# Kernel tuning notes

Hardware: AMD Instinct MI355X
Metric: run time of the kernel (lower is better)

## Reference

```python
import jax, jax.numpy as jnp
import numpy as np

NUM_HEADS = 32
MAX_BIAS_LENGTH = 1024
ROPE_BASE = 10000.0


def _rope_cos_sin(seq_len, head_dim, dtype):
    half = head_dim // 2
    inv_freq = 1.0 / (ROPE_BASE ** (jnp.arange(0, half, dtype=jnp.float32) / half))
    t = jnp.arange(seq_len, dtype=jnp.float32)
    freqs = jnp.outer(t, inv_freq)  # [S, half]
    return jnp.cos(freqs).astype(dtype), jnp.sin(freqs).astype(dtype)


def _apply_rope(x, cos, sin):
    # x: [B, S, H, D]; non-interleaved (GPT-NeoX / flash-attn style) rotary
    half = x.shape[-1] // 2
    x1, x2 = x[..., :half], x[..., half:]
    c = cos[None, :, None, :]
    s = sin[None, :, None, :]
    return jnp.concatenate([x1 * c - x2 * s, x1 * s + x2 * c], axis=-1)


def setup_inputs() -> dict:
    key = jax.random.key(0)
    ks = jax.random.split(key, 7)
    B, S, Dm = 2, 2048, 2048
    std = 1.0 / np.sqrt(Dm)
    return {
        "hidden_states": jax.random.normal(ks[0], (B, S, Dm), jnp.float32),
        "Wq": jax.random.normal(ks[1], (Dm, Dm), jnp.float32) * std,
        "Wk": jax.random.normal(ks[2], (Dm, Dm), jnp.float32) * std,
        "Wv": jax.random.normal(ks[3], (Dm, Dm), jnp.float32) * std,
        "Wo": jax.random.normal(ks[4], (Dm, Dm), jnp.float32) * std,
        "learnable_bias": jax.random.normal(ks[5], (NUM_HEADS, MAX_BIAS_LENGTH), jnp.float32) * 0.001,
        "softmax_offset": jnp.zeros((NUM_HEADS,), jnp.float32),
    }


def reference(hidden_states, Wq, Wk, Wv, Wo, learnable_bias, softmax_offset):
    B, S, Dm = hidden_states.shape
    H = NUM_HEADS
    D = Dm // H
    scale = D ** -0.5

    # projections (nn.Linear: x @ W.T)
    q = (hidden_states @ Wq.T).reshape(B, S, H, D)
    k = (hidden_states @ Wk.T).reshape(B, S, H, D)
    v = (hidden_states @ Wv.T).reshape(B, S, H, D)

    cos, sin = _rope_cos_sin(S, D, q.dtype)
    q = _apply_rope(q, cos, sin)
    k = _apply_rope(k, cos, sin)

    q = q.transpose(0, 2, 1, 3)  # [B, H, S, D]
    k = k.transpose(0, 2, 1, 3)
    v = v.transpose(0, 2, 1, 3)

    scores = jnp.einsum("bhid,bhjd->bhij", q, k) * scale  # [B, H, S, S]

    # per-diagonal learnable bias: diag = i - j in [0, MAX_BIAS_LENGTH)
    i = jnp.arange(S)[:, None]
    j = jnp.arange(S)[None, :]
    diag = i - j  # [S, S]
    causal = diag >= 0
    in_band = causal & (diag < MAX_BIAS_LENGTH)
    bias = jnp.where(in_band, learnable_bias[:, jnp.clip(diag, 0, MAX_BIAS_LENGTH - 1)], 0.0)  # [H, S, S]
    scores = scores + bias[None]
    scores = jnp.where(causal[None, None], scores, -jnp.inf)

    # softmax with learnable per-head offset (attention-sink logit)
    off = softmax_offset[None, :, None]  # [1, H, 1]
    m = jnp.maximum(jnp.max(scores, axis=-1), off)  # [B, H, S]
    p = jnp.exp(scores - m[..., None])
    denom = jnp.sum(p, axis=-1) + jnp.exp(off - m)  # [B, H, S]
    out = jnp.einsum("bhij,bhjd->bhid", p, v) / denom[..., None]

    out = out.transpose(0, 2, 1, 3).reshape(B, S, Dm)
    return out @ Wo.T
```

## Files before the change

kernel.cpp:

```cpp
#include <hip/hip_runtime.h>
#include <hip/hip_bf16.h>
#include <stdint.h>

typedef __bf16 bf16x8 __attribute__((ext_vector_type(8)));
typedef float f32x4 __attribute__((ext_vector_type(4)));
typedef unsigned short u16;
typedef u16 u16x4 __attribute__((ext_vector_type(4)));

#define S_LEN 2048
#define DMODEL 2048
#define NHEADS 32
#define BATCH 2
#define MROWS (BATCH * S_LEN)
#define BIAS_LEN 1024
#define LOG2E 1.44269504088896f

__device__ __forceinline__ u16 b16(float f) {
  union { __bf16 h; u16 u; } cv; cv.h = (__bf16)f; return cv.u;
}

__device__ __forceinline__ void gload16(const void* g, void* l) {
  __builtin_amdgcn_global_load_lds(
      (const __attribute__((address_space(1))) uint32_t*)g,
      (__attribute__((address_space(3))) uint32_t*)l, 16, 0, 0);
}

__global__ __launch_bounds__(256)
void prep_all(const float* __restrict__ hs,
              const float* __restrict__ w0, const float* __restrict__ w1,
              const float* __restrict__ w2, const float* __restrict__ w3,
              const float* __restrict__ bias,
              u16* __restrict__ hs_b, u16* __restrict__ w_b,
              float* __restrict__ ct, float* __restrict__ st,
              u16* __restrict__ b16t)
{
  const int blk = blockIdx.x;
  if (blk < 8192) {
    int i = (blk * 256 + threadIdx.x) * 4;
    float4 v = *(const float4*)(hs + i);
    u16x4 o = { b16(v.x), b16(v.y), b16(v.z), b16(v.w) };
    *(u16x4*)(hs_b + i) = o;
  } else if (blk < 24576) {
    int r = blk - 8192;
    int which = r >> 12;
    const float* src = (which == 0) ? w0 : (which == 1) ? w1
                     : (which == 2) ? w2 : w3;
    int i = ((r & 4095) * 256 + threadIdx.x) * 4;
    float4 v = *(const float4*)(src + i);
    u16x4 o = { b16(v.x), b16(v.y), b16(v.z), b16(v.w) };
    *(u16x4*)(w_b + (size_t)which * DMODEL * DMODEL + i) = o;
  } else if (blk < 24832) {
    int idx = (blk - 24576) * 256 + threadIdx.x;
    int s = idx >> 5, d = idx & 31;
    float inv = exp2f((float)d * (-13.287712379549449f / 32.0f));
    float a = (float)s * inv;
    ct[idx] = cosf(a);
    st[idx] = sinf(a);
  } else {
    int i = (blk - 24832) * 256 + threadIdx.x;
    b16t[i] = b16(bias[i] * LOG2E);
  }
}

#define GEMM_MAIN_LOOP(Aptr, Bptr)                                            \
  f32x4 acc[4][4] = {};                                                       \
  const u16* aS[4]; const u16* bS[4];                                         \
  _Pragma("unroll")                                                           \
  for (int it = 0; it < 4; ++it) {                                            \
    int u = it * 256 + tid;                                                   \
    int row = u >> 3;                                                         \
    int ch  = (u & 7) ^ (row & 7);                                            \
    aS[it] = (Aptr) + (size_t)(tm + row) * DMODEL + ch * 8;                   \
    bS[it] = (Bptr) + (size_t)(tn + row) * DMODEL + ch * 8;                   \
  }                                                                           \
  for (int k0 = 0; k0 < DMODEL; k0 += 64) {                                   \
    __syncthreads();                                                          \
    _Pragma("unroll")                                                         \
    for (int it = 0; it < 4; ++it) {                                          \
      int u = it * 256 + tid;                                                 \
      gload16(aS[it] + k0, (char*)sA + u * 16);                               \
      gload16(bS[it] + k0, (char*)sB + u * 16);                               \
    }                                                                         \
    __syncthreads();                                                          \
    _Pragma("unroll")                                                         \
    for (int kk = 0; kk < 2; ++kk) {                                          \
      bf16x8 af[4], bq[4];                                                    \
      _Pragma("unroll")                                                       \
      for (int mi = 0; mi < 4; ++mi) {                                        \
        int row = wm * 64 + mi * 16 + lc;                                     \
        int ch  = (kk * 4 + lr) ^ (row & 7);                                  \
        af[mi] = *(const bf16x8*)((const char*)sA + row * 128 + ch * 16);     \
      }                                                                       \
      _Pragma("unroll")                                                       \
      for (int ni = 0; ni < 4; ++ni) {                                        \
        int row = wn * 64 + ni * 16 + lc;                                     \
        int ch  = (kk * 4 + lr) ^ (row & 7);                                  \
        bq[ni] = *(const bf16x8*)((const char*)sB + row * 128 + ch * 16);     \
      }                                                                       \
      _Pragma("unroll")                                                       \
      for (int mi = 0; mi < 4; ++mi)                                          \
        _Pragma("unroll")                                                     \
        for (int ni = 0; ni < 4; ++ni)                                        \
          acc[mi][ni] = __builtin_amdgcn_mfma_f32_16x16x32_bf16(              \
              af[mi], bq[ni], acc[mi][ni], 0, 0, 0);                          \
    }                                                                         \
  }

__global__ __launch_bounds__(256)
void gemm_qkv(const u16* __restrict__ A, const u16* __restrict__ W,
              u16* __restrict__ qf, u16* __restrict__ kf, u16* __restrict__ vt,
              const float* __restrict__ ctab, const float* __restrict__ stab)
{
  __shared__ u16 sA[128 * 64];
  __shared__ u16 sB[128 * 64];
  const int tid  = threadIdx.x;
  const int lane = tid & 63;
  const int wid  = tid >> 6;
  const int wm   = wid >> 1, wn = wid & 1;
  const int lc   = lane & 15, lr = lane >> 4;
  const int L = blockIdx.x;
  const int r = L >> 3;
  const int x = (L & 7) * 6 + (r % 6);
  const int y = r / 6;
  const int which = x >> 4;
  const int tn = (x & 15) * 128;
  const int tm = y * 128;
  const u16* Bm = W + (size_t)which * DMODEL * DMODEL;

  GEMM_MAIN_LOOP(A, Bm)

  if (which == 2) {
    u16* C = vt;
#pragma unroll
    for (int mi = 0; mi < 4; ++mi)
#pragma unroll
      for (int ni = 0; ni < 4; ++ni) {
        int col = tn + wn * 64 + ni * 16 + lc;
        int hh = col >> 6, d = col & 63;
        int m0 = tm + wm * 64 + mi * 16 + lr * 4;
        int bb = m0 >> 11, s = m0 & 2047;
        u16x4 v = { b16(acc[mi][ni][0]), b16(acc[mi][ni][1]),
                    b16(acc[mi][ni][2]), b16(acc[mi][ni][3]) };
        *(u16x4*)(C + (((size_t)bb * NHEADS + hh) * 64 + d) * S_LEN + s) = v;
      }
  } else {
    u16* C = (which == 0) ? qf : kf;
    const float scl = (which == 0) ? 0.125f * LOG2E : 1.0f;
#pragma unroll
    for (int mi = 0; mi < 4; ++mi)
#pragma unroll
      for (int ni = 0; ni < 2; ++ni)
#pragma unroll
        for (int j = 0; j < 4; ++j) {
          int col = tn + wn * 64 + ni * 16 + lc;
          int hh = col >> 6, dl = col & 63;
          int rr2 = tm + wm * 64 + mi * 16 + lr * 4 + j;
          int bb = rr2 >> 11, s = rr2 & 2047;
          float x1 = acc[mi][ni][j], x2 = acc[mi][ni + 2][j];
          float cv = ctab[s * 32 + dl], sv = stab[s * 32 + dl];
          float o1 = (x1 * cv - x2 * sv) * scl;
          float o2 = (x1 * sv + x2 * cv) * scl;
          size_t base = (((size_t)bb * NHEADS + hh) * S_LEN + s) * 64 + dl;
          C[base]      = b16(o1);
          C[base + 32] = b16(o2);
        }
  }
}

__global__ __launch_bounds__(256)
void gemm_out(const u16* __restrict__ A, const u16* __restrict__ Bm,
              float* __restrict__ C)
{
  __shared__ u16 sA[128 * 64];
  __shared__ u16 sB[128 * 64];
  const int tid  = threadIdx.x;
  const int lane = tid & 63;
  const int wid  = tid >> 6;
  const int wm   = wid >> 1, wn = wid & 1;
  const int lc   = lane & 15, lr = lane >> 4;
  const int L = blockIdx.x;
  const int r = L >> 3;
  const int x = (L & 7) * 2 + (r & 1);
  const int y = r >> 1;
  const int tn = x * 128;
  const int tm = y * 128;

  GEMM_MAIN_LOOP(A, Bm)

#pragma unroll
  for (int mi = 0; mi < 4; ++mi)
#pragma unroll
    for (int ni = 0; ni < 4; ++ni)
#pragma unroll
      for (int j = 0; j < 4; ++j) {
        int rr2 = tm + wm * 64 + mi * 16 + lr * 4 + j;
        int c = tn + wn * 64 + ni * 16 + lc;
        C[(size_t)rr2 * DMODEL + c] = acc[mi][ni][j];
      }
}

__global__ __launch_bounds__(512, 4)
void attn_kernel(const u16* __restrict__ Q, const u16* __restrict__ K,
                 const u16* __restrict__ V, const u16* __restrict__ bias16,
                 const float* __restrict__ offg, u16* __restrict__ O)
{
  __shared__ __align__(16) u16 sK[2][64 * 64];
  __shared__ __align__(16) u16 sV[2][64 * 64];
  __shared__ __align__(16) u16 sP[16][16 * 72];
  __shared__ __align__(8)  u16 sBiasT[1152];

  const int tid = threadIdx.x, lane = tid & 63, wid = tid >> 6;
  const int lc = lane & 15, lr = lane >> 4;
  const int L  = blockIdx.x;
  const int sidx = L >> 6;
  const int p  = (sidx < 4) ? 7 - sidx : sidx - 4;
  const int bh = L & 63;
  const int h  = bh & 31;
  const int b  = bh >> 5;
  const int qw0 = p * 256 + wid * 16;
  const int nt = 4 * p + 4;

  for (int i = tid; i < 1152; i += 512) {
    int dd = i - 64;
    sBiasT[i] = (dd >= 0 && dd < BIAS_LEN) ? bias16[h * BIAS_LEN + dd] : (u16)0;
  }
  const float off = offg[h] * LOG2E;

  const u16* qp0 = Q + ((size_t)bh * S_LEN + qw0 + lc) * 64;
  bf16x8 aq00 = *(const bf16x8*)(qp0 + lr * 8);
  bf16x8 aq01 = *(const bf16x8*)(qp0 + 32 + lr * 8);
  bf16x8 aq10 = *(const bf16x8*)(qp0 + 128 * 64 + lr * 8);
  bf16x8 aq11 = *(const bf16x8*)(qp0 + 128 * 64 + 32 + lr * 8);

  const int srow = tid >> 3;
  const int sch  = (tid & 7) ^ (srow & 7);
  const u16* kSrc = K + ((size_t)bh * S_LEN + srow) * 64 + sch * 8;
  const u16* vSrc = V + ((size_t)bh * 64 + srow) * S_LEN + sch * 8;

  int offK[4][2], offV[2][4];
#pragma unroll
  for (int f = 0; f < 4; ++f) {
    int row = f * 16 + lc;
    offK[f][0] = row * 128 + ((lr) ^ (row & 7)) * 16;
    offK[f][1] = row * 128 + ((4 + lr) ^ (row & 7)) * 16;
  }
#pragma unroll
  for (int kk = 0; kk < 2; ++kk)
#pragma unroll
    for (int f2 = 0; f2 < 4; ++f2) {
      int drow = f2 * 16 + lc;
      offV[kk][f2] = drow * 128 + ((kk * 4 + lr) ^ (drow & 7)) * 16;
    }

  float lsum0 = 0.0f, lsum1 = 0.0f;
  f32x4 o0[4] = {}, o1[4] = {};

  gload16(kSrc, (char*)sK[0] + tid * 16);
  gload16(vSrc, (char*)sV[0] + tid * 16);
  __syncthreads();

  auto do_group = [&](int dqt, const bf16x8& q0, const bf16x8& q1,
                      u16* myP, float& lsum, const u16* sKc) {
    const int db = dqt + lc;
    const bool inband = (dqt < 1088);
    f32x4 sc[4];
    __builtin_amdgcn_s_setprio(1);
#pragma unroll
    for (int f = 0; f < 4; ++f) {
      f32x4 z;
      if (inband) {
        const int ib = db + 64 - lr * 4 - f * 16;
#pragma unroll
        for (int j = 0; j < 4; ++j)
          z[j] = __uint_as_float((uint32_t)sBiasT[ib - j] << 16);
      } else {
        z[0] = z[1] = z[2] = z[3] = 0.0f;
      }
      bf16x8 k0 = *(const bf16x8*)((const char*)sKc + offK[f][0]);
      bf16x8 k1 = *(const bf16x8*)((const char*)sKc + offK[f][1]);
      z     = __builtin_amdgcn_mfma_f32_16x16x32_bf16(k0, q0, z, 0, 0, 0);
      sc[f] = __builtin_amdgcn_mfma_f32_16x16x32_bf16(k1, q1, z, 0, 0, 0);
    }
    __builtin_amdgcn_s_setprio(0);

    float pvv[4][4];
    if (dqt < 64) {
#pragma unroll
      for (int f = 0; f < 4; ++f)
#pragma unroll
        for (int j = 0; j < 4; ++j) {
          int dd = db - (f * 16 + lr * 4 + j);
          pvv[f][j] = (dd >= 0) ? sc[f][j] : -1e30f;
        }
    } else {
#pragma unroll
      for (int f = 0; f < 4; ++f)
#pragma unroll
        for (int j = 0; j < 4; ++j) pvv[f][j] = sc[f][j];
    }
#pragma unroll
    for (int f = 0; f < 4; ++f)
#pragma unroll
      for (int j = 0; j < 4; ++j) {
        float pe = exp2f(pvv[f][j]);
        pvv[f][j] = pe;
        lsum += pe;
      }
#pragma unroll
    for (int f = 0; f < 4; ++f) {
      u16x4 w = { b16(pvv[f][0]), b16(pvv[f][1]), b16(pvv[f][2]), b16(pvv[f][3]) };
      *(u16x4*)(myP + lc * 72 + f * 16 + lr * 4) = w;
    }
  };

  for (int t = 0; t < nt; ++t) {
    const int cur = t & 1;
    if (t + 1 < nt) {
      gload16(kSrc + (size_t)(t + 1) * 4096, (char*)sK[cur ^ 1] + tid * 16);
      gload16(vSrc + (t + 1) * 64,           (char*)sV[cur ^ 1] + tid * 16);
    }

    const int dqt0 = qw0 - t * 64;
    const int dqt1 = dqt0 + 128;
    const bool a0 = (dqt0 >= 0), a1 = (dqt1 >= 0);

    if (a1) do_group(dqt1, aq10, aq11, sP[wid * 2 + 1], lsum1, sK[cur]);
    if (a0) do_group(dqt0, aq00, aq01, sP[wid * 2 + 0], lsum0, sK[cur]);

    if (a1) {
      asm volatile("s_waitcnt lgkmcnt(0)" ::: "memory");
      __builtin_amdgcn_sched_barrier(0);
      u16* P0 = sP[wid * 2 + 0];
      u16* P1 = sP[wid * 2 + 1];
      __builtin_amdgcn_s_setprio(1);
#pragma unroll
      for (int kk = 0; kk < 2; ++kk) {
        bf16x8 bv[4];
#pragma unroll
        for (int f2 = 0; f2 < 4; ++f2)
          bv[f2] = *(const bf16x8*)((const char*)sV[cur] + offV[kk][f2]);
        bf16x8 ap1 = *(const bf16x8*)(P1 + lc * 72 + kk * 32 + lr * 8);
#pragma unroll
        for (int f2 = 0; f2 < 4; ++f2)
          o1[f2] = __builtin_amdgcn_mfma_f32_16x16x32_bf16(ap1, bv[f2], o1[f2], 0, 0, 0);
        if (a0) {
          bf16x8 ap0 = *(const bf16x8*)(P0 + lc * 72 + kk * 32 + lr * 8);
#pragma unroll
          for (int f2 = 0; f2 < 4; ++f2)
            o0[f2] = __builtin_amdgcn_mfma_f32_16x16x32_bf16(ap0, bv[f2], o0[f2], 0, 0, 0);
        }
      }
      __builtin_amdgcn_s_setprio(0);
    }
    __syncthreads();
  }

  lsum0 += __shfl_xor(lsum0, 16, 64);
  lsum0 += __shfl_xor(lsum0, 32, 64);
  lsum0 += exp2f(off);
  lsum1 += __shfl_xor(lsum1, 16, 64);
  lsum1 += __shfl_xor(lsum1, 32, 64);
  lsum1 += exp2f(off);
  float ls0[4], ls1[4];
#pragma unroll
  for (int j = 0; j < 4; ++j) {
    ls0[j] = 1.0f / __shfl(lsum0, lr * 4 + j, 64);
    ls1[j] = 1.0f / __shfl(lsum1, lr * 4 + j, 64);
  }
#pragma unroll
  for (int f2 = 0; f2 < 4; ++f2)
#pragma unroll
    for (int j = 0; j < 4; ++j) {
      int i0 = qw0 + lr * 4 + j;
      int d = f2 * 16 + lc;
      size_t a0d = (((size_t)(b * S_LEN + i0)) * NHEADS + h) * 64 + d;
      O[a0d] = b16(o0[f2][j] * ls0[j]);
      size_t a1d = (((size_t)(b * S_LEN + i0 + 128)) * NHEADS + h) * 64 + d;
      O[a1d] = b16(o1[f2][j] * ls1[j]);
    }
}

extern "C" void kernel_launch(void* const* d_in, const int* in_sizes, int n_in,
                              void* d_out, int out_size, void* d_ws, size_t ws_size,
                              hipStream_t stream)
{
  const float* hs   = (const float*)d_in[0];
  const float* Wq   = (const float*)d_in[1];
  const float* Wk   = (const float*)d_in[2];
  const float* Wv   = (const float*)d_in[3];
  const float* Wo   = (const float*)d_in[4];
  const float* bias = (const float*)d_in[5];
  const float* off  = (const float*)d_in[6];

  char* p = (char*)d_ws;
  u16* hs_b = (u16*)p; p += (size_t)MROWS * DMODEL * 2;
  u16* wq_b = (u16*)p; p += (size_t)DMODEL * DMODEL * 2;
  u16* wk_b = (u16*)p; p += (size_t)DMODEL * DMODEL * 2;
  u16* wv_b = (u16*)p; p += (size_t)DMODEL * DMODEL * 2;
  u16* wo_b = (u16*)p; p += (size_t)DMODEL * DMODEL * 2;
  u16* qf   = (u16*)p; p += (size_t)MROWS * DMODEL * 2;
  u16* kf   = (u16*)p; p += (size_t)MROWS * DMODEL * 2;
  u16* vt   = (u16*)p; p += (size_t)MROWS * DMODEL * 2;
  u16* att  = (u16*)p; p += (size_t)MROWS * DMODEL * 2;
  float* ct = (float*)p; p += (size_t)S_LEN * 32 * 4;
  float* st = (float*)p; p += (size_t)S_LEN * 32 * 4;
  u16* b16t = (u16*)p; p += (size_t)NHEADS * BIAS_LEN * 2;
  (void)ws_size; (void)in_sizes; (void)n_in; (void)out_size;
  (void)wk_b; (void)wv_b;

  prep_all<<<dim3(24960), 256, 0, stream>>>(hs, Wq, Wk, Wv, Wo, bias,
                                            hs_b, wq_b, ct, st, b16t);
  gemm_qkv<<<dim3(1536), 256, 0, stream>>>(hs_b, wq_b, qf, kf, vt, ct, st);
  attn_kernel<<<dim3(512), 512, 0, stream>>>(qf, kf, vt, b16t, off, att);
  gemm_out<<<dim3(512), 256, 0, stream>>>(att, wo_b, (float*)d_out);
}
```

Measured before the change: 276.3 us.

## Process attention row groups sequentially with a single P buffer per wave

Each of the two query row-groups per wave now runs its full QK, softmax and PV step in turn, reusing one shared P tile per wave instead of two. This halves the sP shared-memory footprint and shortens register live ranges. The launch bound also rises to 6 blocks per SM to allow more resident waves. In exchange, V fragments are reloaded from LDS for each group and the two groups' PV MFMAs no longer interleave, and the tighter register budget could cause spills.

```diff
diff --git a/kernel.cpp b/kernel.cpp
--- a/kernel.cpp
+++ b/kernel.cpp
@@ -199,14 +199,14 @@
       }
 }
 
-__global__ __launch_bounds__(512, 4)
+__global__ __launch_bounds__(512, 6)
 void attn_kernel(const u16* __restrict__ Q, const u16* __restrict__ K,
                  const u16* __restrict__ V, const u16* __restrict__ bias16,
                  const float* __restrict__ offg, u16* __restrict__ O)
 {
   __shared__ __align__(16) u16 sK[2][64 * 64];
   __shared__ __align__(16) u16 sV[2][64 * 64];
-  __shared__ __align__(16) u16 sP[16][16 * 72];
+  __shared__ __align__(16) u16 sP[8][16 * 72];
   __shared__ __align__(8)  u16 sBiasT[1152];
 
   const int tid = threadIdx.x, lane = tid & 63, wid = tid >> 6;
@@ -259,60 +259,6 @@
   gload16(vSrc, (char*)sV[0] + tid * 16);
   __syncthreads();
 
-  auto do_group = [&](int dqt, const bf16x8& q0, const bf16x8& q1,
-                      u16* myP, float& lsum, const u16* sKc) {
-    const int db = dqt + lc;
-    const bool inband = (dqt < 1088);
-    f32x4 sc[4];
-    __builtin_amdgcn_s_setprio(1);
-#pragma unroll
-    for (int f = 0; f < 4; ++f) {
-      f32x4 z;
-      if (inband) {
-        const int ib = db + 64 - lr * 4 - f * 16;
-#pragma unroll
-        for (int j = 0; j < 4; ++j)
-          z[j] = __uint_as_float((uint32_t)sBiasT[ib - j] << 16);
-      } else {
-        z[0] = z[1] = z[2] = z[3] = 0.0f;
-      }
-      bf16x8 k0 = *(const bf16x8*)((const char*)sKc + offK[f][0]);
-      bf16x8 k1 = *(const bf16x8*)((const char*)sKc + offK[f][1]);
-      z     = __builtin_amdgcn_mfma_f32_16x16x32_bf16(k0, q0, z, 0, 0, 0);
-      sc[f] = __builtin_amdgcn_mfma_f32_16x16x32_bf16(k1, q1, z, 0, 0, 0);
-    }
-    __builtin_amdgcn_s_setprio(0);
-
-    float pvv[4][4];
-    if (dqt < 64) {
-#pragma unroll
-      for (int f = 0; f < 4; ++f)
-#pragma unroll
-        for (int j = 0; j < 4; ++j) {
-          int dd = db - (f * 16 + lr * 4 + j);
-          pvv[f][j] = (dd >= 0) ? sc[f][j] : -1e30f;
-        }
-    } else {
-#pragma unroll
-      for (int f = 0; f < 4; ++f)
-#pragma unroll
-        for (int j = 0; j < 4; ++j) pvv[f][j] = sc[f][j];
-    }
-#pragma unroll
-    for (int f = 0; f < 4; ++f)
-#pragma unroll
-      for (int j = 0; j < 4; ++j) {
-        float pe = exp2f(pvv[f][j]);
-        pvv[f][j] = pe;
-        lsum += pe;
-      }
-#pragma unroll
-    for (int f = 0; f < 4; ++f) {
-      u16x4 w = { b16(pvv[f][0]), b16(pvv[f][1]), b16(pvv[f][2]), b16(pvv[f][3]) };
-      *(u16x4*)(myP + lc * 72 + f * 16 + lr * 4) = w;
-    }
-  };
-
   for (int t = 0; t < nt; ++t) {
     const int cur = t & 1;
     if (t + 1 < nt) {
@@ -321,34 +267,82 @@
     }
 
     const int dqt0 = qw0 - t * 64;
-    const int dqt1 = dqt0 + 128;
-    const bool a0 = (dqt0 >= 0), a1 = (dqt1 >= 0);
-
-    if (a1) do_group(dqt1, aq10, aq11, sP[wid * 2 + 1], lsum1, sK[cur]);
-    if (a0) do_group(dqt0, aq00, aq01, sP[wid * 2 + 0], lsum0, sK[cur]);
-
-    if (a1) {
+    u16* myP = sP[wid];
+
+#pragma unroll
+    for (int g = 1; g >= 0; --g) {
+      const int dqt = dqt0 + g * 128;
+      if (dqt < 0) continue;
+      const bf16x8 q0 = g ? aq10 : aq00;
+      const bf16x8 q1 = g ? aq11 : aq01;
+      f32x4* o = g ? o1 : o0;
+      float& lsum = g ? lsum1 : lsum0;
+
+      const int db = dqt + lc;
+      const bool inband = (dqt < 1088);
+      f32x4 sc[4];
+      __builtin_amdgcn_s_setprio(1);
+#pragma unroll
+      for (int f = 0; f < 4; ++f) {
+        f32x4 z;
+        if (inband) {
+          const int ib = db + 64 - lr * 4 - f * 16;
+#pragma unroll
+          for (int j = 0; j < 4; ++j)
+            z[j] = __uint_as_float((uint32_t)sBiasT[ib - j] << 16);
+        } else {
+          z[0] = z[1] = z[2] = z[3] = 0.0f;
+        }
+        bf16x8 k0 = *(const bf16x8*)((const char*)sK[cur] + offK[f][0]);
+        bf16x8 k1 = *(const bf16x8*)((const char*)sK[cur] + offK[f][1]);
+        z     = __builtin_amdgcn_mfma_f32_16x16x32_bf16(k0, q0, z, 0, 0, 0);
+        sc[f] = __builtin_amdgcn_mfma_f32_16x16x32_bf16(k1, q1, z, 0, 0, 0);
+      }
+      __builtin_amdgcn_s_setprio(0);
+
+      float pvv[4][4];
+      if (dqt < 64) {
+#pragma unroll
+        for (int f = 0; f < 4; ++f)
+#pragma unroll
+          for (int j = 0; j < 4; ++j) {
+            int dd = db - (f * 16 + lr * 4 + j);
+            pvv[f][j] = (dd >= 0) ? sc[f][j] : -1e30f;
+          }
+      } else {
+#pragma unroll
+        for (int f = 0; f < 4; ++f)
+#pragma unroll
+          for (int j = 0; j < 4; ++j) pvv[f][j] = sc[f][j];
+      }
+#pragma unroll
+      for (int f = 0; f < 4; ++f)
+#pragma unroll
+        for (int j = 0; j < 4; ++j) {
+          float pe = exp2f(pvv[f][j]);
+          pvv[f][j] = pe;
+          lsum += pe;
+        }
+
+#pragma unroll
+      for (int f = 0; f < 4; ++f) {
+        u16x4 w = { b16(pvv[f][0]), b16(pvv[f][1]), b16(pvv[f][2]), b16(pvv[f][3]) };
+        *(u16x4*)(myP + lc * 72 + f * 16 + lr * 4) = w;
+      }
       asm volatile("s_waitcnt lgkmcnt(0)" ::: "memory");
       __builtin_amdgcn_sched_barrier(0);
-      u16* P0 = sP[wid * 2 + 0];
-      u16* P1 = sP[wid * 2 + 1];
+      bf16x8 ap0 = *(const bf16x8*)(myP + lc * 72 + lr * 8);
+      bf16x8 ap1 = *(const bf16x8*)(myP + lc * 72 + 32 + lr * 8);
       __builtin_amdgcn_s_setprio(1);
 #pragma unroll
-      for (int kk = 0; kk < 2; ++kk) {
-        bf16x8 bv[4];
-#pragma unroll
-        for (int f2 = 0; f2 < 4; ++f2)
-          bv[f2] = *(const bf16x8*)((const char*)sV[cur] + offV[kk][f2]);
-        bf16x8 ap1 = *(const bf16x8*)(P1 + lc * 72 + kk * 32 + lr * 8);
-#pragma unroll
-        for (int f2 = 0; f2 < 4; ++f2)
-          o1[f2] = __builtin_amdgcn_mfma_f32_16x16x32_bf16(ap1, bv[f2], o1[f2], 0, 0, 0);
-        if (a0) {
-          bf16x8 ap0 = *(const bf16x8*)(P0 + lc * 72 + kk * 32 + lr * 8);
-#pragma unroll
-          for (int f2 = 0; f2 < 4; ++f2)
-            o0[f2] = __builtin_amdgcn_mfma_f32_16x16x32_bf16(ap0, bv[f2], o0[f2], 0, 0, 0);
-        }
+      for (int f2 = 0; f2 < 4; ++f2) {
+        bf16x8 bv = *(const bf16x8*)((const char*)sV[cur] + offV[0][f2]);
+        o[f2] = __builtin_amdgcn_mfma_f32_16x16x32_bf16(ap0, bv, o[f2], 0, 0, 0);
+      }
+#pragma unroll
+      for (int f2 = 0; f2 < 4; ++f2) {
+        bf16x8 bv = *(const bf16x8*)((const char*)sV[cur] + offV[1][f2]);
+        o[f2] = __builtin_amdgcn_mfma_f32_16x16x32_bf16(ap1, bv, o[f2], 0, 0, 0);
       }
       __builtin_amdgcn_s_setprio(0);
     }
```

New measurement: 314.1 us. 13.7% more time.
